# Kernel optimization log

Hardware: AMD Instinct MI355X
Metric: run time of the kernel (lower is better)

Reference implementation:

```python
import jax, jax.numpy as jnp
import numpy as np

B, T, C, H = 2, 2048, 1024, 16
D = C // H  # head dim = 64


def setup_inputs() -> dict:
    key = jax.random.key(0)
    ks = jax.random.split(key, 9)
    s = 1.0 / np.sqrt(C)
    x = jax.random.normal(ks[0], (B, T, C), dtype=jnp.float32)
    # causal lower-triangular mask, broadcast over heads: [B, 1, T, T]
    attn_mask = jnp.broadcast_to(jnp.tril(jnp.ones((T, T), dtype=jnp.int32)), (B, 1, T, T))
    Wq = jax.random.normal(ks[1], (C, C), dtype=jnp.float32) * s
    Wk = jax.random.normal(ks[2], (C, C), dtype=jnp.float32) * s
    Wv = jax.random.normal(ks[3], (C, C), dtype=jnp.float32) * s
    Wo = jax.random.normal(ks[4], (C, C), dtype=jnp.float32) * s
    bq = jax.random.normal(ks[5], (C,), dtype=jnp.float32) * s
    bk = jax.random.normal(ks[6], (C,), dtype=jnp.float32) * s
    bv = jax.random.normal(ks[7], (C,), dtype=jnp.float32) * s
    bo = jax.random.normal(ks[8], (C,), dtype=jnp.float32) * s
    return {"x": x, "attn_mask": attn_mask, "Wq": Wq, "bq": bq, "Wk": Wk, "bk": bk,
            "Wv": Wv, "bv": bv, "Wo": Wo, "bo": bo}


def reference(x, attn_mask, Wq, bq, Wk, bk, Wv, bv, Wo, bo):
    # Q/K/V projections: nn.Linear applies x @ W^T + b
    def split_heads(t):  # [B,T,C] -> [B,H,T,D]
        return t.reshape(B, T, H, D).transpose(0, 2, 1, 3)

    q = split_heads(x @ Wq.T + bq)
    k = split_heads(x @ Wk.T + bk)
    v = split_heads(x @ Wv.T + bv)

    scale = 1.0 / np.sqrt(D)
    att = jnp.einsum('bhqd,bhkd->bhqk', q, k) * scale  # [B,H,T,T]
    att = jnp.where(attn_mask[:, :, :T, :T] == 0, -jnp.inf, att)
    att = jax.nn.softmax(att, axis=-1)
    # dropout p=0.0 -> identity
    y = jnp.einsum('bhqk,bhkd->bhqd', att, v)  # [B,H,T,D]
    y = y.transpose(0, 2, 1, 3).reshape(B, T, C)
    return y @ Wo.T + bo
```

## Files before the change

### kernel.cpp

```cpp
#include <hip/hip_runtime.h>
#include <hip/hip_bf16.h>

#define B_ 2
#define T_ 2048
#define C_ 1024
#define H_ 16
#define D_ 64
#define BT_ (B_ * T_)
#define S3_ 3072

typedef __bf16 bf16x8 __attribute__((ext_vector_type(8)));
typedef short short8 __attribute__((ext_vector_type(8)));
typedef float f32x4 __attribute__((ext_vector_type(4)));

__device__ inline bf16x8 ld_frag_bf(const short* p) {
    short8 s = *(const short8*)p;
    return __builtin_bit_cast(bf16x8, s);
}
__device__ inline short f2bf(float f) {
    union { float f; unsigned u; } x;
    x.f = f;
    unsigned r = x.u + 0x7fff + ((x.u >> 16) & 1);
    return (short)(r >> 16);
}
__device__ inline void st_out(short* p, float v) { *p = f2bf(v); }
__device__ inline void st_out(float* p, float v) { *p = v; }

__device__ inline void async16(const void* g, void* l) {
    __builtin_amdgcn_global_load_lds(
        (const __attribute__((address_space(1))) unsigned*)g,
        (__attribute__((address_space(3))) unsigned*)l, 16, 0, 0);
}

__global__ __launch_bounds__(256) void conv_inputs(
    const float* __restrict__ x,
    const float* __restrict__ Wq, const float* __restrict__ Wk,
    const float* __restrict__ Wv, const float* __restrict__ Wo,
    short* __restrict__ xb, short* __restrict__ Wqkvb, short* __restrict__ Wob)
{
    size_t e = ((size_t)blockIdx.x * 256 + threadIdx.x) * 8;
    int r = (int)(e >> 20);
    size_t off = e & ((1u << 20) - 1);
    const float* src; short* dst;
    if (r < 4)      { src = x + e;  dst = xb + e; }
    else if (r < 7) { src = (r == 4 ? Wq : r == 5 ? Wk : Wv) + off;
                      dst = Wqkvb + ((size_t)(r - 4) << 20) + off; }
    else            { src = Wo + off; dst = Wob + off; }
    f32x4 a = *(const f32x4*)src;
    f32x4 b = *(const f32x4*)(src + 4);
    short8 s;
#pragma unroll
    for (int i = 0; i < 4; ++i) { s[i] = f2bf(a[i]); s[i + 4] = f2bf(b[i]); }
    *(short8*)dst = s;
}

template <typename OT>
__global__ __launch_bounds__(256) void gemm_m97(
    const short* __restrict__ A, int lda,
    const short* __restrict__ Wb,
    const float* __restrict__ b0, const float* __restrict__ b1,
    const float* __restrict__ b2,
    OT* __restrict__ Out, int ldo)
{
    constexpr int K = 1024;
    __shared__ __align__(16) short Bs[128 * 32];
    __shared__ __align__(16) short As[128 * 32];

    const int tid = threadIdx.x;
    const int w = tid >> 6, l = tid & 63;
    const int c = l & 15, qd = l >> 4;
    const int m0 = blockIdx.y * 128, n0 = blockIdx.x * 128;
    const int wm = w >> 1, wn = w & 1;

    const float* bias = (n0 < 1024) ? b0 : (n0 < 2048 ? b1 : b2);

    f32x4 acc[4][4] = {};

    for (int k0 = 0; k0 < K; k0 += 32) {
#pragma unroll
        for (int p = 0; p < 2; ++p) {
            int row = p * 64 + w * 16 + (l >> 2);
            async16(Wb + (size_t)(n0 + row) * K + k0 + (l & 3) * 8,
                    Bs + p * 2048 + w * 512 + l * 8);
            async16(A + (size_t)(m0 + row) * lda + k0 + (l & 3) * 8,
                    As + p * 2048 + w * 512 + l * 8);
        }
        __syncthreads();

        bf16x8 af[4], bfr[4];
#pragma unroll
        for (int i = 0; i < 4; ++i) {
            af[i]  = ld_frag_bf(As + (wm * 64 + i * 16 + c) * 32 + qd * 8);
            bfr[i] = ld_frag_bf(Bs + (wn * 64 + i * 16 + c) * 32 + qd * 8);
        }
#pragma unroll
        for (int i = 0; i < 4; ++i)
#pragma unroll
            for (int j = 0; j < 4; ++j)
                acc[i][j] = __builtin_amdgcn_mfma_f32_16x16x32_bf16(af[i], bfr[j], acc[i][j], 0, 0, 0);
        __syncthreads();
    }

#pragma unroll
    for (int i = 0; i < 4; ++i)
#pragma unroll
        for (int j = 0; j < 4; ++j) {
            int n = n0 + wn * 64 + j * 16 + c;
            float bv = bias[n & 1023];
#pragma unroll
            for (int r = 0; r < 4; ++r) {
                int m = m0 + wm * 64 + i * 16 + qd * 4 + r;
                st_out(Out + (size_t)m * ldo + n, acc[i][j][r] + bv);
            }
        }
}

template <typename OT>
__global__ __launch_bounds__(256) void gemm_n64(
    const short* __restrict__ A, int lda,
    const short* __restrict__ Wb, const float* __restrict__ bias,
    OT* __restrict__ Out, int ldo)
{
    constexpr int K = 1024;
    __shared__ __align__(16) short Bs[64 * 32];
    __shared__ __align__(16) short As[128 * 32];

    const int tid = threadIdx.x;
    const int w = tid >> 6, l = tid & 63;
    const int c = l & 15, qd = l >> 4;
    const int m0 = blockIdx.y * 128, n0 = blockIdx.x * 64;
    const int wm = w >> 1, wn = w & 1;

    f32x4 acc[4][2] = {};

    for (int k0 = 0; k0 < K; k0 += 32) {
        {
            int row = w * 16 + (l >> 2);
            async16(Wb + (size_t)(n0 + row) * K + k0 + (l & 3) * 8,
                    Bs + w * 512 + l * 8);
        }
#pragma unroll
        for (int p = 0; p < 2; ++p) {
            int row = p * 64 + w * 16 + (l >> 2);
            async16(A + (size_t)(m0 + row) * lda + k0 + (l & 3) * 8,
                    As + p * 2048 + w * 512 + l * 8);
        }
        __syncthreads();

        bf16x8 af[4], bfr[2];
#pragma unroll
        for (int i = 0; i < 4; ++i)
            af[i] = ld_frag_bf(As + (wm * 64 + i * 16 + c) * 32 + qd * 8);
#pragma unroll
        for (int j = 0; j < 2; ++j)
            bfr[j] = ld_frag_bf(Bs + (wn * 32 + j * 16 + c) * 32 + qd * 8);
#pragma unroll
        for (int i = 0; i < 4; ++i)
#pragma unroll
            for (int j = 0; j < 2; ++j)
                acc[i][j] = __builtin_amdgcn_mfma_f32_16x16x32_bf16(af[i], bfr[j], acc[i][j], 0, 0, 0);
        __syncthreads();
    }

#pragma unroll
    for (int i = 0; i < 4; ++i)
#pragma unroll
        for (int j = 0; j < 2; ++j) {
            int n = n0 + wn * 32 + j * 16 + c;
            float bv = bias[n];
#pragma unroll
            for (int r = 0; r < 4; ++r) {
                int m = m0 + wm * 64 + i * 16 + qd * 4 + r;
                st_out(Out + (size_t)m * ldo + n, acc[i][j][r] + bv);
            }
        }
}

__global__ __launch_bounds__(256) void transpose_v(
    const short* __restrict__ QKV, short* __restrict__ VT)
{
    __shared__ short Tm[64 * 80];
    const int t = threadIdx.x;
    const int kt = blockIdx.x, bh = blockIdx.y;
    const int b = bh >> 4, h = bh & 15;
    const short* Vg = QKV + (size_t)b * T_ * S3_ + 2048 + h * 64;

    {
        int key = t >> 2, dc = (t & 3) * 16;
        const short* g = Vg + (size_t)(kt * 64 + key) * S3_ + dc;
        short8 a = *(const short8*)g;
        short8 c8 = *(const short8*)(g + 8);
#pragma unroll
        for (int e = 0; e < 8; ++e) {
            Tm[(dc + e) * 80 + key]     = a[e];
            Tm[(dc + 8 + e) * 80 + key] = c8[e];
        }
    }
    __syncthreads();
    {
        int d = t >> 2, kc = (t & 3) * 16;
        short8 w0 = *(const short8*)&Tm[d * 80 + kc];
        short8 w1 = *(const short8*)&Tm[d * 80 + kc + 8];
        short* o = VT + ((size_t)bh * 64 + d) * T_ + kt * 64 + kc;
        *(short8*)o = w0;
        *(short8*)(o + 8) = w1;
    }
}

__global__ __launch_bounds__(256) void attn_flash5(
    short* __restrict__ QKV, const short* __restrict__ VT)
{
    __shared__ __align__(16) short Ksm[2][64 * 64];
    __shared__ __align__(16) short Vsm[2][64 * 64];
    __shared__ __align__(16) short Psm[4][16 * 72];

    const int tid = threadIdx.x;
    const int w = tid >> 6, l = tid & 63;
    const int c = l & 15, qd = l >> 4;
    const int id = blockIdx.x;
    const int bh = (id & 7) * 4 + ((id >> 3) & 3);
    const int pair = id >> 5;
    const int b = bh >> 4, h = bh & 15;
    const int sw = c & 7;

    short* Qbase = QKV + (size_t)b * T_ * S3_ + h * 64;
    const short* Kbase = Qbase + 1024;
    const short* VTb = VT + (size_t)bh * 64 * T_;

#pragma unroll 1
    for (int seg = 0; seg < 2; ++seg) {
        const int qt = seg ? (31 - pair) : pair;
        const int wq0 = qt * 64 + w * 16;

        bf16x8 aq0 = ld_frag_bf(Qbase + (size_t)(wq0 + c) * S3_ + qd * 8);
        bf16x8 aq1 = ld_frag_bf(Qbase + (size_t)(wq0 + c) * S3_ + 32 + qd * 8);

        f32x4 o[4] = {};
        float lrow[4] = {0.f, 0.f, 0.f, 0.f};

#pragma unroll
        for (int p = 0; p < 2; ++p) {
            int row = p * 32 + w * 8 + (l >> 3);
            int srcC = (l & 7) ^ (row & 7);
            async16(Kbase + (size_t)row * S3_ + srcC * 8,
                    &Ksm[0][row * 64 + (l & 7) * 8]);
            async16(VTb + (size_t)row * T_ + srcC * 8,
                    &Vsm[0][row * 64 + (l & 7) * 8]);
        }
        __syncthreads();

#pragma unroll 1
        for (int kt = 0; kt <= qt; ++kt) {
            const int cur = kt & 1;
            const int k0 = kt * 64;

            if (kt < qt) {
#pragma unroll
                for (int p = 0; p < 2; ++p) {
                    int row = p * 32 + w * 8 + (l >> 3);
                    int srcC = (l & 7) ^ (row & 7);
                    async16(Kbase + (size_t)(k0 + 64 + row) * S3_ + srcC * 8,
                            &Ksm[1 - cur][row * 64 + (l & 7) * 8]);
                    async16(VTb + (size_t)row * T_ + k0 + 64 + srcC * 8,
                            &Vsm[1 - cur][row * 64 + (l & 7) * 8]);
                }
            }

            f32x4 s[4];
#pragma unroll
            for (int j = 0; j < 4; ++j) {
                s[j] = (f32x4){0.f, 0.f, 0.f, 0.f};
                const short* kr = &Ksm[cur][(j * 16 + c) * 64];
                bf16x8 kb0 = ld_frag_bf(kr + (qd ^ sw) * 8);
                bf16x8 kb1 = ld_frag_bf(kr + ((qd ^ 4) ^ sw) * 8);
                s[j] = __builtin_amdgcn_mfma_f32_16x16x32_bf16(aq0, kb0, s[j], 0, 0, 0);
                s[j] = __builtin_amdgcn_mfma_f32_16x16x32_bf16(aq1, kb1, s[j], 0, 0, 0);
            }

            float p_[4][4];
            if (kt < qt) {
#pragma unroll
                for (int r = 0; r < 4; ++r) {
                    float acc = 0.f;
#pragma unroll
                    for (int j = 0; j < 4; ++j) {
                        float p = __expf(fmaf(s[j][r], 0.125f, -8.0f));
                        p_[r][j] = p;
                        acc += p;
                    }
                    lrow[r] += acc;
                }
            } else {
#pragma unroll
                for (int r = 0; r < 4; ++r) {
                    const int qrow = wq0 + qd * 4 + r;
                    float acc = 0.f;
#pragma unroll
                    for (int j = 0; j < 4; ++j) {
                        float p = __expf(fmaf(s[j][r], 0.125f, -8.0f));
                        if (k0 + j * 16 + c > qrow) p = 0.f;
                        p_[r][j] = p;
                        acc += p;
                    }
                    lrow[r] += acc;
                }
            }

            short* P = Psm[w];
#pragma unroll
            for (int r = 0; r < 4; ++r)
#pragma unroll
                for (int j = 0; j < 4; ++j)
                    P[(qd * 4 + r) * 72 + j * 16 + c] = f2bf(p_[r][j]);

            bf16x8 pa0 = ld_frag_bf(P + c * 72 + qd * 8);
            bf16x8 pa1 = ld_frag_bf(P + c * 72 + 32 + qd * 8);
#pragma unroll
            for (int j = 0; j < 4; ++j) {
                const short* vr = &Vsm[cur][(j * 16 + c) * 64];
                bf16x8 vb0 = ld_frag_bf(vr + (qd ^ sw) * 8);
                bf16x8 vb1 = ld_frag_bf(vr + ((qd ^ 4) ^ sw) * 8);
                o[j] = __builtin_amdgcn_mfma_f32_16x16x32_bf16(pa0, vb0, o[j], 0, 0, 0);
                o[j] = __builtin_amdgcn_mfma_f32_16x16x32_bf16(pa1, vb1, o[j], 0, 0, 0);
            }
            __syncthreads();
        }

        float inv[4];
#pragma unroll
        for (int r = 0; r < 4; ++r) {
            float s = lrow[r];
            s += __shfl_xor(s, 1);
            s += __shfl_xor(s, 2);
            s += __shfl_xor(s, 4);
            s += __shfl_xor(s, 8);
            inv[r] = 1.0f / s;
        }

#pragma unroll
        for (int j = 0; j < 4; ++j)
#pragma unroll
            for (int r = 0; r < 4; ++r) {
                int qrow = wq0 + qd * 4 + r;
                Qbase[(size_t)qrow * S3_ + j * 16 + c] = f2bf(o[j][r] * inv[r]);
            }
    }
}

extern "C" void kernel_launch(void* const* d_in, const int* in_sizes, int n_in,
                              void* d_out, int out_size, void* d_ws, size_t ws_size,
                              hipStream_t stream)
{
    const float* x  = (const float*)d_in[0];
    const float* Wq = (const float*)d_in[2];
    const float* bq = (const float*)d_in[3];
    const float* Wk = (const float*)d_in[4];
    const float* bk = (const float*)d_in[5];
    const float* Wv = (const float*)d_in[6];
    const float* bv = (const float*)d_in[7];
    const float* Wo = (const float*)d_in[8];
    const float* bo = (const float*)d_in[9];
    float* out = (float*)d_out;

    short* QKVs  = (short*)d_ws;
    short* Wqkvb = QKVs + (size_t)BT_ * S3_;
    short* Wob   = Wqkvb + (size_t)S3_ * C_;
    short* xb    = (short*)d_out;
    short* VT    = (short*)d_out + (size_t)4 * 1024 * 1024;

    conv_inputs<<<4096, 256, 0, stream>>>(x, Wq, Wk, Wv, Wo, xb, Wqkvb, Wob);
    gemm_m97<short><<<dim3(S3_ / 128, BT_ / 128), 256, 0, stream>>>(
        xb, C_, Wqkvb, bq, bk, bv, QKVs, S3_);
    transpose_v<<<dim3(T_ / 64, B_ * H_), 256, 0, stream>>>(QKVs, VT);
    attn_flash5<<<512, 256, 0, stream>>>(QKVs, VT);
    gemm_n64<float><<<dim3(C_ / 64, BT_ / 128), 256, 0, stream>>>(
        QKVs, S3_, Wob, bo, out, C_);
}
```

Measured before the change: 210.4 us.

## Fuse V transpose into QKV GEMM epilogue and keep P in registers

```diff
diff --git a/kernel.cpp b/kernel.cpp
--- a/kernel.cpp
+++ b/kernel.cpp
@@ -10,11 +10,12 @@
 #define S3_ 3072
 
 typedef __bf16 bf16x8 __attribute__((ext_vector_type(8)));
-typedef short short8 __attribute__((ext_vector_type(8)));
+typedef short short8v __attribute__((ext_vector_type(8)));
+typedef short s16x4 __attribute__((ext_vector_type(4)));
 typedef float f32x4 __attribute__((ext_vector_type(4)));
 
 __device__ inline bf16x8 ld_frag_bf(const short* p) {
-    short8 s = *(const short8*)p;
+    short8v s = *(const short8v*)p;
     return __builtin_bit_cast(bf16x8, s);
 }
 __device__ inline short f2bf(float f) {
@@ -48,19 +49,18 @@
     else            { src = Wo + off; dst = Wob + off; }
     f32x4 a = *(const f32x4*)src;
     f32x4 b = *(const f32x4*)(src + 4);
-    short8 s;
+    short8v s;
 #pragma unroll
     for (int i = 0; i < 4; ++i) { s[i] = f2bf(a[i]); s[i + 4] = f2bf(b[i]); }
-    *(short8*)dst = s;
-}
-
-template <typename OT>
-__global__ __launch_bounds__(256) void gemm_m97(
-    const short* __restrict__ A, int lda,
+    *(short8v*)dst = s;
+}
+
+__global__ __launch_bounds__(256) void gemm_qkv(
+    const short* __restrict__ A,
     const short* __restrict__ Wb,
     const float* __restrict__ b0, const float* __restrict__ b1,
     const float* __restrict__ b2,
-    OT* __restrict__ Out, int ldo)
+    short* __restrict__ Out, short* __restrict__ VQ)
 {
     constexpr int K = 1024;
     __shared__ __align__(16) short Bs[128 * 32];
@@ -72,8 +72,6 @@
     const int m0 = blockIdx.y * 128, n0 = blockIdx.x * 128;
     const int wm = w >> 1, wn = w & 1;
 
-    const float* bias = (n0 < 1024) ? b0 : (n0 < 2048 ? b1 : b2);
-
     f32x4 acc[4][4] = {};
 
     for (int k0 = 0; k0 < K; k0 += 32) {
@@ -82,7 +80,7 @@
             int row = p * 64 + w * 16 + (l >> 2);
             async16(Wb + (size_t)(n0 + row) * K + k0 + (l & 3) * 8,
                     Bs + p * 2048 + w * 512 + l * 8);
-            async16(A + (size_t)(m0 + row) * lda + k0 + (l & 3) * 8,
+            async16(A + (size_t)(m0 + row) * K + k0 + (l & 3) * 8,
                     As + p * 2048 + w * 512 + l * 8);
         }
         __syncthreads();
@@ -101,18 +99,36 @@
         __syncthreads();
     }
 
-#pragma unroll
-    for (int i = 0; i < 4; ++i)
-#pragma unroll
-        for (int j = 0; j < 4; ++j) {
-            int n = n0 + wn * 64 + j * 16 + c;
-            float bv = bias[n & 1023];
-#pragma unroll
-            for (int r = 0; r < 4; ++r) {
-                int m = m0 + wm * 64 + i * 16 + qd * 4 + r;
-                st_out(Out + (size_t)m * ldo + n, acc[i][j][r] + bv);
-            }
-        }
+    if (n0 >= 2048) {
+        const int h  = (n0 - 2048 + wn * 64) >> 6;
+        const int b  = m0 >> 11;
+        const int kt = ((m0 & 2047) + wm * 64) >> 6;
+        short* vt = VQ + (((size_t)(b * 16 + h) * 32 + kt) * 4096);
+#pragma unroll
+        for (int i = 0; i < 4; ++i)
+#pragma unroll
+            for (int j = 0; j < 4; ++j) {
+                float bv = b2[n0 - 2048 + wn * 64 + j * 16 + c];
+                s16x4 st;
+#pragma unroll
+                for (int r = 0; r < 4; ++r) st[r] = f2bf(acc[i][j][r] + bv);
+                *(s16x4*)&vt[((i * 4 + j) * 64 + qd * 16 + c) * 4] = st;
+            }
+    } else {
+        const float* bias = (n0 < 1024) ? b0 : b1;
+#pragma unroll
+        for (int i = 0; i < 4; ++i)
+#pragma unroll
+            for (int j = 0; j < 4; ++j) {
+                int n = n0 + wn * 64 + j * 16 + c;
+                float bv = bias[n & 1023];
+#pragma unroll
+                for (int r = 0; r < 4; ++r) {
+                    int m = m0 + wm * 64 + i * 16 + qd * 4 + r;
+                    Out[(size_t)m * S3_ + n] = f2bf(acc[i][j][r] + bv);
+                }
+            }
+    }
 }
 
 template <typename OT>
@@ -176,43 +192,11 @@
         }
 }
 
-__global__ __launch_bounds__(256) void transpose_v(
-    const short* __restrict__ QKV, short* __restrict__ VT)
-{
-    __shared__ short Tm[64 * 80];
-    const int t = threadIdx.x;
-    const int kt = blockIdx.x, bh = blockIdx.y;
-    const int b = bh >> 4, h = bh & 15;
-    const short* Vg = QKV + (size_t)b * T_ * S3_ + 2048 + h * 64;
-
-    {
-        int key = t >> 2, dc = (t & 3) * 16;
-        const short* g = Vg + (size_t)(kt * 64 + key) * S3_ + dc;
-        short8 a = *(const short8*)g;
-        short8 c8 = *(const short8*)(g + 8);
-#pragma unroll
-        for (int e = 0; e < 8; ++e) {
-            Tm[(dc + e) * 80 + key]     = a[e];
-            Tm[(dc + 8 + e) * 80 + key] = c8[e];
-        }
-    }
-    __syncthreads();
-    {
-        int d = t >> 2, kc = (t & 3) * 16;
-        short8 w0 = *(const short8*)&Tm[d * 80 + kc];
-        short8 w1 = *(const short8*)&Tm[d * 80 + kc + 8];
-        short* o = VT + ((size_t)bh * 64 + d) * T_ + kt * 64 + kc;
-        *(short8*)o = w0;
-        *(short8*)(o + 8) = w1;
-    }
-}
-
-__global__ __launch_bounds__(256) void attn_flash5(
-    short* __restrict__ QKV, const short* __restrict__ VT)
-{
-    __shared__ __align__(16) short Ksm[2][64 * 64];
-    __shared__ __align__(16) short Vsm[2][64 * 64];
-    __shared__ __align__(16) short Psm[4][16 * 72];
+__global__ __launch_bounds__(256) void attn_flash6(
+    short* __restrict__ QKV, const short* __restrict__ VQ)
+{
+    __shared__ __align__(16) short Ksm[2][4096];
+    __shared__ __align__(16) short Vsm[2][4096];
 
     const int tid = threadIdx.x;
     const int w = tid >> 6, l = tid & 63;
@@ -225,7 +209,7 @@
 
     short* Qbase = QKV + (size_t)b * T_ * S3_ + h * 64;
     const short* Kbase = Qbase + 1024;
-    const short* VTb = VT + (size_t)bh * 64 * T_;
+    const short* VTb = VQ + (size_t)bh * 32 * 4096;
 
 #pragma unroll 1
     for (int seg = 0; seg < 2; ++seg) {
@@ -236,7 +220,7 @@
         bf16x8 aq1 = ld_frag_bf(Qbase + (size_t)(wq0 + c) * S3_ + 32 + qd * 8);
 
         f32x4 o[4] = {};
-        float lrow[4] = {0.f, 0.f, 0.f, 0.f};
+        float lsum = 0.f;
 
 #pragma unroll
         for (int p = 0; p < 2; ++p) {
@@ -244,8 +228,8 @@
             int srcC = (l & 7) ^ (row & 7);
             async16(Kbase + (size_t)row * S3_ + srcC * 8,
                     &Ksm[0][row * 64 + (l & 7) * 8]);
-            async16(VTb + (size_t)row * T_ + srcC * 8,
-                    &Vsm[0][row * 64 + (l & 7) * 8]);
+            async16(VTb + p * 2048 + w * 512 + l * 8,
+                    &Vsm[0][p * 2048 + w * 512 + l * 8]);
         }
         __syncthreads();
 
@@ -255,95 +239,74 @@
             const int k0 = kt * 64;
 
             if (kt < qt) {
+                const short* vtile = VTb + (size_t)(kt + 1) * 4096;
 #pragma unroll
                 for (int p = 0; p < 2; ++p) {
                     int row = p * 32 + w * 8 + (l >> 3);
                     int srcC = (l & 7) ^ (row & 7);
                     async16(Kbase + (size_t)(k0 + 64 + row) * S3_ + srcC * 8,
                             &Ksm[1 - cur][row * 64 + (l & 7) * 8]);
-                    async16(VTb + (size_t)row * T_ + k0 + 64 + srcC * 8,
-                            &Vsm[1 - cur][row * 64 + (l & 7) * 8]);
+                    async16(vtile + p * 2048 + w * 512 + l * 8,
+                            &Vsm[1 - cur][p * 2048 + w * 512 + l * 8]);
                 }
             }
 
-            f32x4 s[4];
+            f32x4 st[4];
 #pragma unroll
             for (int j = 0; j < 4; ++j) {
-                s[j] = (f32x4){0.f, 0.f, 0.f, 0.f};
+                st[j] = (f32x4){0.f, 0.f, 0.f, 0.f};
                 const short* kr = &Ksm[cur][(j * 16 + c) * 64];
                 bf16x8 kb0 = ld_frag_bf(kr + (qd ^ sw) * 8);
                 bf16x8 kb1 = ld_frag_bf(kr + ((qd ^ 4) ^ sw) * 8);
-                s[j] = __builtin_amdgcn_mfma_f32_16x16x32_bf16(aq0, kb0, s[j], 0, 0, 0);
-                s[j] = __builtin_amdgcn_mfma_f32_16x16x32_bf16(aq1, kb1, s[j], 0, 0, 0);
-            }
-
-            float p_[4][4];
+                st[j] = __builtin_amdgcn_mfma_f32_16x16x32_bf16(kb0, aq0, st[j], 0, 0, 0);
+                st[j] = __builtin_amdgcn_mfma_f32_16x16x32_bf16(kb1, aq1, st[j], 0, 0, 0);
+            }
+
+            s16x4 pb[4];
             if (kt < qt) {
 #pragma unroll
-                for (int r = 0; r < 4; ++r) {
-                    float acc = 0.f;
-#pragma unroll
-                    for (int j = 0; j < 4; ++j) {
-                        float p = __expf(fmaf(s[j][r], 0.125f, -8.0f));
-                        p_[r][j] = p;
-                        acc += p;
+                for (int j = 0; j < 4; ++j)
+#pragma unroll
+                    for (int r = 0; r < 4; ++r) {
+                        float p = __expf(fmaf(st[j][r], 0.125f, -8.0f));
+                        lsum += p;
+                        pb[j][r] = f2bf(p);
                     }
-                    lrow[r] += acc;
+            } else {
+                const int qloc = w * 16 + c;
+#pragma unroll
+                for (int j = 0; j < 4; ++j)
+#pragma unroll
+                    for (int r = 0; r < 4; ++r) {
+                        float p = __expf(fmaf(st[j][r], 0.125f, -8.0f));
+                        if (j * 16 + qd * 4 + r > qloc) p = 0.f;
+                        lsum += p;
+                        pb[j][r] = f2bf(p);
+                    }
+            }
+
+#pragma unroll
+            for (int j = 0; j < 4; ++j)
+#pragma unroll
+                for (int i = 0; i < 4; ++i) {
+                    s16x4 vf = *(const s16x4*)&Vsm[cur][((j * 4 + i) * 64 + qd * 16 + c) * 4];
+                    o[i] = __builtin_amdgcn_mfma_f32_16x16x16bf16_1k(vf, pb[j], o[i], 0, 0, 0);
                 }
-            } else {
-#pragma unroll
-                for (int r = 0; r < 4; ++r) {
-                    const int qrow = wq0 + qd * 4 + r;
-                    float acc = 0.f;
-#pragma unroll
-                    for (int j = 0; j < 4; ++j) {
-                        float p = __expf(fmaf(s[j][r], 0.125f, -8.0f));
-                        if (k0 + j * 16 + c > qrow) p = 0.f;
-                        p_[r][j] = p;
-                        acc += p;
-                    }
-                    lrow[r] += acc;
-                }
-            }
-
-            short* P = Psm[w];
-#pragma unroll
-            for (int r = 0; r < 4; ++r)
-#pragma unroll
-                for (int j = 0; j < 4; ++j)
-                    P[(qd * 4 + r) * 72 + j * 16 + c] = f2bf(p_[r][j]);
-
-            bf16x8 pa0 = ld_frag_bf(P + c * 72 + qd * 8);
-            bf16x8 pa1 = ld_frag_bf(P + c * 72 + 32 + qd * 8);
-#pragma unroll
-            for (int j = 0; j < 4; ++j) {
-                const short* vr = &Vsm[cur][(j * 16 + c) * 64];
-                bf16x8 vb0 = ld_frag_bf(vr + (qd ^ sw) * 8);
-                bf16x8 vb1 = ld_frag_bf(vr + ((qd ^ 4) ^ sw) * 8);
-                o[j] = __builtin_amdgcn_mfma_f32_16x16x32_bf16(pa0, vb0, o[j], 0, 0, 0);
-                o[j] = __builtin_amdgcn_mfma_f32_16x16x32_bf16(pa1, vb1, o[j], 0, 0, 0);
-            }
             __syncthreads();
         }
 
-        float inv[4];
-#pragma unroll
-        for (int r = 0; r < 4; ++r) {
-            float s = lrow[r];
-            s += __shfl_xor(s, 1);
-            s += __shfl_xor(s, 2);
-            s += __shfl_xor(s, 4);
-            s += __shfl_xor(s, 8);
-            inv[r] = 1.0f / s;
-        }
-
-#pragma unroll
-        for (int j = 0; j < 4; ++j)
-#pragma unroll
-            for (int r = 0; r < 4; ++r) {
-                int qrow = wq0 + qd * 4 + r;
-                Qbase[(size_t)qrow * S3_ + j * 16 + c] = f2bf(o[j][r] * inv[r]);
-            }
+        float lt = lsum;
+        lt += __shfl_xor(lt, 16);
+        lt += __shfl_xor(lt, 32);
+        float inv = 1.0f / lt;
+
+#pragma unroll
+        for (int i = 0; i < 4; ++i) {
+            s16x4 yb;
+#pragma unroll
+            for (int r = 0; r < 4; ++r) yb[r] = f2bf(o[i][r] * inv);
+            *(s16x4*)&Qbase[(size_t)(wq0 + c) * S3_ + i * 16 + qd * 4] = yb;
+        }
     }
 }
 
@@ -366,13 +329,12 @@
     short* Wqkvb = QKVs + (size_t)BT_ * S3_;
     short* Wob   = Wqkvb + (size_t)S3_ * C_;
     short* xb    = (short*)d_out;
-    short* VT    = (short*)d_out + (size_t)4 * 1024 * 1024;
+    short* VQ    = (short*)d_out + (size_t)4 * 1024 * 1024;
 
     conv_inputs<<<4096, 256, 0, stream>>>(x, Wq, Wk, Wv, Wo, xb, Wqkvb, Wob);
-    gemm_m97<short><<<dim3(S3_ / 128, BT_ / 128), 256, 0, stream>>>(
-        xb, C_, Wqkvb, bq, bk, bv, QKVs, S3_);
-    transpose_v<<<dim3(T_ / 64, B_ * H_), 256, 0, stream>>>(QKVs, VT);
-    attn_flash5<<<512, 256, 0, stream>>>(QKVs, VT);
+    gemm_qkv<<<dim3(S3_ / 128, BT_ / 128), 256, 0, stream>>>(
+        xb, Wqkvb, bq, bk, bv, QKVs, VQ);
+    attn_flash6<<<512, 256, 0, stream>>>(QKVs, VQ);
     gemm_n64<float><<<dim3(C_ / 64, BT_ / 128), 256, 0, stream>>>(
         QKVs, S3_, Wob, bo, out, C_);
 }
```

New measurement: 217.9 us. 3.6% more time.
